# Performance work log

Hardware: AMD Instinct MI355X
Metric: run time of the kernel (lower is better)

The kernel has to match this reference:

```python
import jax, jax.numpy as jnp
import numpy as np

D_MODEL = 1024
N_HEADS = 16
HEAD_DIM = D_MODEL // N_HEADS
EPS = 1e-8  # torch F.cosine_similarity eps


def setup_inputs() -> dict:
    key = jax.random.key(0)
    ks = jax.random.split(key, 5)
    B, S = 2, 2048
    scale = 1.0 / np.sqrt(D_MODEL)
    return {
        "x": jax.random.normal(ks[0], (B, S, D_MODEL), dtype=jnp.float32),
        "W_q": jax.random.normal(ks[1], (D_MODEL, D_MODEL), dtype=jnp.float32) * scale,
        "W_k": jax.random.normal(ks[2], (D_MODEL, D_MODEL), dtype=jnp.float32) * scale,
        "W_v": jax.random.normal(ks[3], (D_MODEL, D_MODEL), dtype=jnp.float32) * scale,
        "W_o": jax.random.normal(ks[4], (D_MODEL, D_MODEL), dtype=jnp.float32) * scale,
    }


def _split_heads(t, B, S):
    # [B,S,D] -> [B,H,S,hd]
    return t.reshape(B, S, N_HEADS, HEAD_DIM).transpose(0, 2, 1, 3)


def reference(x, W_q, W_k, W_v, W_o):
    B, S, _ = x.shape
    Q = _split_heads(x @ W_q.T, B, S)
    K = _split_heads(x @ W_k.T, B, S)
    V = _split_heads(x @ W_v.T, B, S)

    # score[b,h,i,j] = cos_sim(q_i*k_j, ones) = sum_d(q*k) / (||q*k|| * sqrt(hd))
    num = jnp.einsum("bhid,bhjd->bhij", Q, K)
    # ||q_i \odot k_j||^2 = sum_d q^2 k^2, computed as a GEMM (no [B,H,S,S,D] blowup)
    norm_sq = jnp.einsum("bhid,bhjd->bhij", Q * Q, K * K)
    denom = jnp.maximum(jnp.sqrt(norm_sq), EPS) * jnp.sqrt(jnp.float32(HEAD_DIM))
    attn_scores = num / denom

    attn_weights = jax.nn.softmax(attn_scores, axis=-1)
    out = jnp.einsum("bhij,bhjd->bhid", attn_weights, V)
    out = out.transpose(0, 2, 1, 3).reshape(B, S, D_MODEL)
    out = out @ W_o.T
    return out, attn_weights
```

## Files before the change

### kernel.cpp

```cpp
#include <hip/hip_runtime.h>
#include <stdint.h>

typedef __bf16 bf16_t;
typedef __bf16 bf16x4_t __attribute__((ext_vector_type(4)));
typedef __bf16 bf16x8_t __attribute__((ext_vector_type(8)));
typedef float  f32x4_t  __attribute__((ext_vector_type(4)));

#define S_LEN 2048
#define DMODEL 1024
#define NHEAD 16
#define HDIM 64
#define MTOT 4096
#define NT 32
#define WBLK 4864

__device__ __forceinline__ f32x4_t mfma16(bf16x8_t a, bf16x8_t b, f32x4_t c){
  return __builtin_amdgcn_mfma_f32_16x16x32_bf16(a, b, c, 0, 0, 0);
}

__device__ __forceinline__ void gload_lds16(const bf16_t* g, bf16_t* l){
  __builtin_amdgcn_global_load_lds(
      (const __attribute__((address_space(1))) void*)(uintptr_t)g,
      (__attribute__((address_space(3))) void*)(uintptr_t)l,
      16, 0, 0);
}

template<int ROWS>
__device__ __forceinline__ void stage_tile(bf16_t* lds, const bf16_t* __restrict__ g,
                                           int ldg, int wid, int lane){
  const int rl = lane >> 3;
  const int cs = ((lane & 7) ^ rl) << 3;
#pragma unroll
  for (int it = 0; it < ROWS/32; ++it){
    const int chunk = it*4 + wid;
    gload_lds16(g + (size_t)(chunk*8 + rl)*ldg + cs, lds + chunk*512);
  }
}

__device__ __forceinline__ void stage_slice16(bf16_t* lds, const bf16_t* __restrict__ g,
                                              int lane){
  const int rl = lane >> 3;
  const int cs = ((lane & 7) ^ rl) << 3;
#pragma unroll
  for (int c = 0; c < 2; ++c)
    gload_lds16(g + (size_t)(c*8 + rl)*HDIM + cs, lds + c*512);
}

__device__ __forceinline__ void stage_v(bf16_t* lds, const bf16_t* __restrict__ g,
                                        int lane){
#pragma unroll
  for (int c = 0; c < 2; ++c)
    gload_lds16(g + (size_t)lane*64 + c*8, lds + c*512);
}

__device__ __forceinline__ bf16x8_t lds_read8(const bf16_t* t, int row, int ko){
  return *(const bf16x8_t*)&t[row*64 + (ko ^ ((row & 7) << 3))];
}

__device__ __forceinline__ bf16x8_t sq8(bf16x8_t v){
  bf16x8_t r;
#pragma unroll
  for (int i=0;i<8;i++){ float f = (float)v[i]; r[i] = (bf16_t)(f*f); }
  return r;
}

__global__ __launch_bounds__(256)
void vsa_cast_kernel(const float* __restrict__ src, bf16_t* __restrict__ dst, int n4){
  int i = blockIdx.x*256 + threadIdx.x;
  if (i >= n4) return;
  float4 v = ((const float4*)src)[i];
  bf16x4_t o = {(bf16_t)v.x,(bf16_t)v.y,(bf16_t)v.z,(bf16_t)v.w};
  ((bf16x4_t*)dst)[i] = o;
}

__global__ __launch_bounds__(256)
void vsa_qkv_kernel(const bf16_t* __restrict__ xb, const bf16_t* __restrict__ Wb,
                    bf16_t* __restrict__ Qb, bf16_t* __restrict__ Kb,
                    bf16_t* __restrict__ Vblk)
{
  __shared__ __align__(16) bf16_t Ah[128][64], Bh[128][64];
  const int z  = blockIdx.z;
  const int m0 = blockIdx.x * 128;
  const int n0 = blockIdx.y * 128;
  const int tid = threadIdx.x, lane = tid & 63, wid = tid >> 6;
  const int wr = (wid >> 1) * 64, wc = (wid & 1) * 64;
  const bf16_t* Wz = Wb + (size_t)z * (DMODEL*DMODEL);

  const f32x4_t zz = {0.f,0.f,0.f,0.f};
  f32x4_t acc[4][4];
#pragma unroll
  for (int i=0;i<4;i++)
#pragma unroll
    for (int j=0;j<4;j++) acc[i][j] = zz;

  for (int kt = 0; kt < 16; ++kt){
    const int k0 = kt * 64;
    stage_tile<128>(&Ah[0][0], xb + (size_t)m0*DMODEL + k0, DMODEL, wid, lane);
    stage_tile<128>(&Bh[0][0], Wz + (size_t)n0*DMODEL + k0, DMODEL, wid, lane);
    __syncthreads();
#pragma unroll
    for (int kk = 0; kk < 2; ++kk){
      const int ko = kk*32 + (lane>>4)*8;
      bf16x8_t ah[4], bh4[4];
#pragma unroll
      for (int i=0;i<4;i++){
        ah[i]  = lds_read8(&Ah[0][0], wr + i*16 + (lane&15), ko);
        bh4[i] = lds_read8(&Bh[0][0], wc + i*16 + (lane&15), ko);
      }
#pragma unroll
      for (int i=0;i<4;i++)
#pragma unroll
        for (int j=0;j<4;j++)
          acc[i][j] = mfma16(ah[i], bh4[j], acc[i][j]);
    }
    __syncthreads();
  }

#pragma unroll
  for (int i=0;i<4;i++)
#pragma unroll
    for (int j=0;j<4;j++)
#pragma unroll
      for (int r=0;r<4;r++){
        const int m = m0 + wr + i*16 + ((lane>>4)<<2) + r;
        const int n = n0 + wc + j*16 + (lane&15);
        const float q = acc[i][j][r];
        const int b = m >> 11, s = m & 2047, h = n >> 6, d = n & 63;
        const size_t bh_ = (size_t)b*NHEAD + h;
        if (z == 0){
          Qb[(bh_*S_LEN + s)*HDIM + d] = (bf16_t)q;
        } else if (z == 1){
          Kb[(bh_*S_LEN + s)*HDIM + d] = (bf16_t)q;
        } else {
          Vblk[bh_*(size_t)(S_LEN*HDIM) + (size_t)(s>>6)*4096 + d*64 + (s&63)] = (bf16_t)q;
        }
      }
}

__global__ __launch_bounds__(256, 4)
void vsa_attn_kernel(const bf16_t* __restrict__ Qb,
                     const bf16_t* __restrict__ Kb,
                     const bf16_t* __restrict__ Vblk,
                     float* __restrict__ Wout,
                     bf16_t* __restrict__ o1)
{
  __shared__ __align__(16) bf16_t smem[4*WBLK];
  __shared__ float lred[4][2][16];

  const int lin = blockIdx.x;
  const int xcd = lin & 7;
  const int idx = lin >> 3;
  const int qt  = idx & 63;
  const int bh  = xcd + 8*(idx >> 6);
  const int lane = threadIdx.x & 63, w = (int)(threadIdx.x >> 6);
  const int qr = lane & 15, cg = lane >> 4;

  const size_t base = (size_t)bh * (S_LEN*HDIM);
  const bf16_t* Kg = Kb   + base + (size_t)(w*16)*HDIM;
  const bf16_t* Vg = Vblk + base + w*16;

  bf16_t* Kbuf = smem + w*WBLK;
  bf16_t* Vbuf = Kbuf + 2048;
  bf16_t* Pbuf = Vbuf + 2048;

  bf16x8_t aq[2][2], aq2[2][2];
#pragma unroll
  for (int qh = 0; qh < 2; ++qh){
    const bf16_t* qrow = Qb + base + (size_t)(qt*32 + qh*16 + qr)*HDIM;
#pragma unroll
    for (int kk = 0; kk < 2; ++kk){
      aq[qh][kk] = *(const bf16x8_t*)(qrow + kk*32 + cg*8);
      bf16x8_t t;
#pragma unroll
      for (int e=0;e<8;e++){ float f = (float)aq[qh][kk][e]; t[e] = (bf16_t)(64.f*f*f); }
      aq2[qh][kk] = t;
    }
  }

  float lp[2][4] = {{0.f,0.f,0.f,0.f},{0.f,0.f,0.f,0.f}};
  stage_slice16(Kbuf, Kg, lane);
  for (int jt = 0; jt < NT; ++jt){
    const int nb = (jt+1) & (NT-1);
    __builtin_amdgcn_sched_barrier(0);
    stage_slice16(Kbuf + ((jt+1)&1)*1024, Kg + (size_t)nb*64*HDIM, lane);
    asm volatile("s_waitcnt vmcnt(2)" ::: "memory");
    __builtin_amdgcn_sched_barrier(0);
    const bf16_t* kb = Kbuf + (jt&1)*1024;
    bf16x8_t kf0  = lds_read8(kb, qr, cg*8), kf1 = lds_read8(kb, qr, 32+cg*8);
    bf16x8_t k2f0 = sq8(kf0),                k2f1 = sq8(kf1);
    f32x4_t nu[2], nr[2];
    __builtin_amdgcn_s_setprio(1);
#pragma unroll
    for (int qh = 0; qh < 2; ++qh){
      f32x4_t a = {0.f,0.f,0.f,0.f}, b = {0.f,0.f,0.f,0.f};
      a = mfma16(aq[qh][0],  kf0,  a); a = mfma16(aq[qh][1],  kf1,  a);
      b = mfma16(aq2[qh][0], k2f0, b); b = mfma16(aq2[qh][1], k2f1, b);
      nu[qh] = a; nr[qh] = b;
    }
    __builtin_amdgcn_s_setprio(0);
#pragma unroll
    for (int qh = 0; qh < 2; ++qh)
#pragma unroll
      for (int r=0;r<4;r++){
        const float s = nu[qh][r]*rsqrtf(fmaxf(nr[qh][r], 6.4e-15f));
        lp[qh][r] += __expf(s);
      }
  }

#pragma unroll
  for (int qh=0;qh<2;qh++)
#pragma unroll
    for (int r=0;r<4;r++){
      float l = lp[qh][r];
      l += __shfl_xor(l,1); l += __shfl_xor(l,2);
      l += __shfl_xor(l,4); l += __shfl_xor(l,8);
      lred[w][qh][cg*4+r] = l;
    }
  __syncthreads();
  float rl[2][4];
#pragma unroll
  for (int qh=0;qh<2;qh++)
#pragma unroll
    for (int r=0;r<4;r++)
      rl[qh][r] = 1.0f/(lred[0][qh][cg*4+r]+lred[1][qh][cg*4+r]
                       +lred[2][qh][cg*4+r]+lred[3][qh][cg*4+r]);

  const f32x4_t zz = {0.f,0.f,0.f,0.f};
  f32x4_t oacc[2][4];
#pragma unroll
  for (int qh=0;qh<2;qh++)
#pragma unroll
    for (int n=0;n<4;n++) oacc[qh][n] = zz;
  const size_t wb = (size_t)bh * S_LEN * S_LEN;
  const bf16x8_t zero8 = {};

  stage_v(Vbuf, Vg, lane);
  asm volatile("s_waitcnt vmcnt(0)" ::: "memory");
  __builtin_amdgcn_sched_barrier(0);

  for (int jt = 0; jt < NT; ++jt){
    const int nb = (jt+1) & (NT-1);
    __builtin_amdgcn_sched_barrier(0);
    stage_slice16(Kbuf + ((jt+1)&1)*1024, Kg + (size_t)nb*64*HDIM, lane);
    stage_v(Vbuf + ((jt+1)&1)*1024, Vg + (size_t)nb*4096, lane);
    asm volatile("s_waitcnt vmcnt(12)" ::: "memory");
    __builtin_amdgcn_sched_barrier(0);
    const bf16_t* kb = Kbuf + (jt&1)*1024;
    bf16x8_t kf0  = lds_read8(kb, qr, cg*8), kf1 = lds_read8(kb, qr, 32+cg*8);
    bf16x8_t k2f0 = sq8(kf0),                k2f1 = sq8(kf1);
    f32x4_t nu[2], nr[2];
    __builtin_amdgcn_s_setprio(1);
#pragma unroll
    for (int qh = 0; qh < 2; ++qh){
      f32x4_t a = {0.f,0.f,0.f,0.f}, b = {0.f,0.f,0.f,0.f};
      a = mfma16(aq[qh][0],  kf0,  a); a = mfma16(aq[qh][1],  kf1,  a);
      b = mfma16(aq2[qh][0], k2f0, b); b = mfma16(aq2[qh][1], k2f1, b);
      nu[qh] = a; nr[qh] = b;
    }
    __builtin_amdgcn_s_setprio(0);
#pragma unroll
    for (int qh = 0; qh < 2; ++qh)
#pragma unroll
      for (int r=0;r<4;r++){
        const float s = nu[qh][r]*rsqrtf(fmaxf(nr[qh][r], 6.4e-15f));
        const float wgt = __expf(s) * rl[qh][r];
        const int i = qt*32 + qh*16 + cg*4 + r;
        const int j = jt*64 + w*16 + qr;
        Wout[wb + (size_t)i*S_LEN + j] = wgt;
        Pbuf[qh*384 + (cg*4+r)*24 + qr] = (bf16_t)wgt;
      }
    asm volatile("s_waitcnt lgkmcnt(0)" ::: "memory");
    __builtin_amdgcn_sched_barrier(0);
    const int k0 = (cg & 1) * 8;
    bf16x8_t pa0 = (cg < 2) ? *(const bf16x8_t*)&Pbuf[      qr*24 + k0] : zero8;
    bf16x8_t pa1 = (cg < 2) ? *(const bf16x8_t*)&Pbuf[384 + qr*24 + k0] : zero8;
    const bf16_t* vbase = Vbuf + (jt&1)*1024 + (cg&1)*512;
    __builtin_amdgcn_s_setprio(1);
#pragma unroll
    for (int n=0;n<4;n++){
      bf16x8_t vb = *(const bf16x8_t*)&vbase[(n*16+qr)*8];
      oacc[0][n] = mfma16(pa0, vb, oacc[0][n]);
      oacc[1][n] = mfma16(pa1, vb, oacc[1][n]);
    }
    __builtin_amdgcn_s_setprio(0);
  }

  asm volatile("s_waitcnt vmcnt(0)" ::: "memory");
  __builtin_amdgcn_sched_barrier(0);
  float* Ow = (float*)Kbuf;
#pragma unroll
  for (int qh=0;qh<2;qh++)
#pragma unroll
    for (int n=0;n<4;n++)
#pragma unroll
      for (int r=0;r<4;r++)
        Ow[(qh*16+cg*4+r)*68 + n*16+qr] = oacc[qh][n][r];
  __syncthreads();
  {
    const int row = lane >> 1;
    const int jl  = (lane & 1)*8;
    float v[8];
#pragma unroll
    for (int e=0;e<8;e++) v[e] = 0.f;
#pragma unroll
    for (int ww=0; ww<4; ++ww){
      const float* Os = (const float*)(smem + ww*WBLK);
#pragma unroll
      for (int e=0;e<8;e++) v[e] += Os[row*68 + w*16 + jl + e];
    }
    const int b = bh >> 4, h = bh & 15;
    const int srow = qt*32 + row;
    const size_t o = ((size_t)b*S_LEN + srow)*DMODEL + (size_t)h*HDIM + w*16 + jl;
    bf16x8_t hv;
#pragma unroll
    for (int e=0;e<8;e++) hv[e] = (bf16_t)v[e];
    *(bf16x8_t*)(o1 + o) = hv;
  }
}

__global__ __launch_bounds__(256)
void vsa_oproj_kernel(const bf16_t* __restrict__ Ab, const bf16_t* __restrict__ Bb,
                      float* __restrict__ out)
{
  __shared__ __align__(16) bf16_t Ah[64][64], Bh[128][64];
  const int m0 = blockIdx.x * 64;
  const int n0 = blockIdx.y * 128;
  const int tid = threadIdx.x, lane = tid & 63, wid = tid >> 6;
  const int wc = wid * 32;

  const f32x4_t zz = {0.f,0.f,0.f,0.f};
  f32x4_t acc[4][2];
#pragma unroll
  for (int i=0;i<4;i++)
#pragma unroll
    for (int j=0;j<2;j++) acc[i][j] = zz;

  for (int kt = 0; kt < 16; ++kt){
    const int k0 = kt * 64;
    stage_tile<64> (&Ah[0][0], Ab + (size_t)m0*DMODEL + k0, DMODEL, wid, lane);
    stage_tile<128>(&Bh[0][0], Bb + (size_t)n0*DMODEL + k0, DMODEL, wid, lane);
    __syncthreads();
#pragma unroll
    for (int kk = 0; kk < 2; ++kk){
      const int ko = kk*32 + (lane>>4)*8;
      bf16x8_t ah[4], bh4[2];
#pragma unroll
      for (int i=0;i<4;i++)
        ah[i] = lds_read8(&Ah[0][0], i*16 + (lane&15), ko);
#pragma unroll
      for (int j=0;j<2;j++)
        bh4[j] = lds_read8(&Bh[0][0], wc + j*16 + (lane&15), ko);
#pragma unroll
      for (int i=0;i<4;i++)
#pragma unroll
        for (int j=0;j<2;j++)
          acc[i][j] = mfma16(ah[i], bh4[j], acc[i][j]);
    }
    __syncthreads();
  }

#pragma unroll
  for (int i=0;i<4;i++)
#pragma unroll
    for (int j=0;j<2;j++)
#pragma unroll
      for (int r=0;r<4;r++){
        const int m = m0 + i*16 + ((lane>>4)<<2) + r;
        const int n = n0 + wc + j*16 + (lane&15);
        out[(size_t)m*DMODEL + n] = acc[i][j][r];
      }
}

extern "C" void kernel_launch(void* const* d_in, const int* in_sizes, int n_in,
                              void* d_out, int out_size, void* d_ws, size_t ws_size,
                              hipStream_t stream)
{
  const float* x  = (const float*)d_in[0];
  const float* Wq = (const float*)d_in[1];
  const float* Wk = (const float*)d_in[2];
  const float* Wv = (const float*)d_in[3];
  const float* Wo = (const float*)d_in[4];
  float* out  = (float*)d_out;
  float* attw = out + (size_t)MTOT*DMODEL;

  bf16_t* ws = (bf16_t*)d_ws;
  const size_t C = 4194304;
  bf16_t* xb   = ws;
  bf16_t* Wb   = ws + C;
  bf16_t* Qb   = ws + 2*C;
  bf16_t* Kb   = ws + 3*C;
  bf16_t* Vblk = ws + 4*C;
  bf16_t* o1   = ws + 5*C;

  const int W1 = DMODEL*DMODEL;
  vsa_cast_kernel<<<(int)(C/1024), 256, 0, stream>>>(x,  xb, (int)(C/4));
  vsa_cast_kernel<<<W1/1024, 256, 0, stream>>>(Wq, Wb + 0*(size_t)W1, W1/4);
  vsa_cast_kernel<<<W1/1024, 256, 0, stream>>>(Wk, Wb + 1*(size_t)W1, W1/4);
  vsa_cast_kernel<<<W1/1024, 256, 0, stream>>>(Wv, Wb + 2*(size_t)W1, W1/4);
  vsa_cast_kernel<<<W1/1024, 256, 0, stream>>>(Wo, Wb + 3*(size_t)W1, W1/4);

  vsa_qkv_kernel<<<dim3(32, 8, 3), 256, 0, stream>>>(xb, Wb, Qb, Kb, Vblk);
  vsa_attn_kernel<<<dim3(2048), 256, 0, stream>>>(Qb, Kb, Vblk, attw, o1);
  vsa_oproj_kernel<<<dim3(64, 8), 256, 0, stream>>>(o1, Wb + 3*(size_t)W1, out);
}
```

Baseline: 308.7 us.

## Transpose score MFMA operands to vectorize weight stores and simplify row-sum reduction

Swaps the A/B operands of the score MFMAs so each lane holds four consecutive key columns for a single query row. The attention-weight output can then be written as 16-byte float4 stores and the P tile as 8-byte bf16x4 stores, instead of scattered scalar writes. The row-sum reduction shrinks to two cross-lane shuffles. Softmax normalization is folded into the exponent as exp2(s*log2e - log2(sum)), and the vmcnt wait threshold is adjusted to match the new number of outstanding loads. The risks are a small change in rounding and getting the wait count wrong for the new store pattern.

```diff
diff --git a/kernel.cpp b/kernel.cpp
--- a/kernel.cpp
+++ b/kernel.cpp
@@ -13,6 +13,7 @@
 #define MTOT 4096
 #define NT 32
 #define WBLK 4864
+#define LOG2E 1.4426950408889634f
 
 __device__ __forceinline__ f32x4_t mfma16(bf16x8_t a, bf16x8_t b, f32x4_t c){
   return __builtin_amdgcn_mfma_f32_16x16x32_bf16(a, b, c, 0, 0, 0);
@@ -177,7 +178,7 @@
     }
   }
 
-  float lp[2][4] = {{0.f,0.f,0.f,0.f},{0.f,0.f,0.f,0.f}};
+  float lp[2] = {0.f, 0.f};
   stage_slice16(Kbuf, Kg, lane);
   for (int jt = 0; jt < NT; ++jt){
     const int nb = (jt+1) & (NT-1);
@@ -193,8 +194,8 @@
 #pragma unroll
     for (int qh = 0; qh < 2; ++qh){
       f32x4_t a = {0.f,0.f,0.f,0.f}, b = {0.f,0.f,0.f,0.f};
-      a = mfma16(aq[qh][0],  kf0,  a); a = mfma16(aq[qh][1],  kf1,  a);
-      b = mfma16(aq2[qh][0], k2f0, b); b = mfma16(aq2[qh][1], k2f1, b);
+      a = mfma16(kf0,  aq[qh][0],  a); a = mfma16(kf1,  aq[qh][1],  a);
+      b = mfma16(k2f0, aq2[qh][0], b); b = mfma16(k2f1, aq2[qh][1], b);
       nu[qh] = a; nr[qh] = b;
     }
     __builtin_amdgcn_s_setprio(0);
@@ -203,27 +204,23 @@
 #pragma unroll
       for (int r=0;r<4;r++){
         const float s = nu[qh][r]*rsqrtf(fmaxf(nr[qh][r], 6.4e-15f));
-        lp[qh][r] += __expf(s);
+        lp[qh] += __builtin_amdgcn_exp2f(s * LOG2E);
       }
   }
 
 #pragma unroll
-  for (int qh=0;qh<2;qh++)
-#pragma unroll
-    for (int r=0;r<4;r++){
-      float l = lp[qh][r];
-      l += __shfl_xor(l,1); l += __shfl_xor(l,2);
-      l += __shfl_xor(l,4); l += __shfl_xor(l,8);
-      lred[w][qh][cg*4+r] = l;
-    }
+  for (int qh=0;qh<2;qh++){
+    float l = lp[qh];
+    l += __shfl_xor(l,16); l += __shfl_xor(l,32);
+    lred[w][qh][qr] = l;
+  }
   __syncthreads();
-  float rl[2][4];
-#pragma unroll
-  for (int qh=0;qh<2;qh++)
-#pragma unroll
-    for (int r=0;r<4;r++)
-      rl[qh][r] = 1.0f/(lred[0][qh][cg*4+r]+lred[1][qh][cg*4+r]
-                       +lred[2][qh][cg*4+r]+lred[3][qh][cg*4+r]);
+  float lrl2[2];
+#pragma unroll
+  for (int qh=0;qh<2;qh++){
+    const float lsum = lred[0][qh][qr]+lred[1][qh][qr]+lred[2][qh][qr]+lred[3][qh][qr];
+    lrl2[qh] = -__log2f(lsum);
+  }
 
   const f32x4_t zz = {0.f,0.f,0.f,0.f};
   f32x4_t oacc[2][4];
@@ -243,7 +240,7 @@
     __builtin_amdgcn_sched_barrier(0);
     stage_slice16(Kbuf + ((jt+1)&1)*1024, Kg + (size_t)nb*64*HDIM, lane);
     stage_v(Vbuf + ((jt+1)&1)*1024, Vg + (size_t)nb*4096, lane);
-    asm volatile("s_waitcnt vmcnt(12)" ::: "memory");
+    asm volatile("s_waitcnt vmcnt(6)" ::: "memory");
     __builtin_amdgcn_sched_barrier(0);
     const bf16_t* kb = Kbuf + (jt&1)*1024;
     bf16x8_t kf0  = lds_read8(kb, qr, cg*8), kf1 = lds_read8(kb, qr, 32+cg*8);
@@ -253,22 +250,24 @@
 #pragma unroll
     for (int qh = 0; qh < 2; ++qh){
       f32x4_t a = {0.f,0.f,0.f,0.f}, b = {0.f,0.f,0.f,0.f};
-      a = mfma16(aq[qh][0],  kf0,  a); a = mfma16(aq[qh][1],  kf1,  a);
-      b = mfma16(aq2[qh][0], k2f0, b); b = mfma16(aq2[qh][1], k2f1, b);
+      a = mfma16(kf0,  aq[qh][0],  a); a = mfma16(kf1,  aq[qh][1],  a);
+      b = mfma16(k2f0, aq2[qh][0], b); b = mfma16(k2f1, aq2[qh][1], b);
       nu[qh] = a; nr[qh] = b;
     }
     __builtin_amdgcn_s_setprio(0);
 #pragma unroll
-    for (int qh = 0; qh < 2; ++qh)
+    for (int qh = 0; qh < 2; ++qh){
+      f32x4_t wv;
 #pragma unroll
       for (int r=0;r<4;r++){
         const float s = nu[qh][r]*rsqrtf(fmaxf(nr[qh][r], 6.4e-15f));
-        const float wgt = __expf(s) * rl[qh][r];
-        const int i = qt*32 + qh*16 + cg*4 + r;
-        const int j = jt*64 + w*16 + qr;
-        Wout[wb + (size_t)i*S_LEN + j] = wgt;
-        Pbuf[qh*384 + (cg*4+r)*24 + qr] = (bf16_t)wgt;
+        wv[r] = __builtin_amdgcn_exp2f(__builtin_fmaf(s, LOG2E, lrl2[qh]));
       }
+      *(f32x4_t*)(Wout + wb + (size_t)(qt*32 + qh*16 + qr)*S_LEN
+                  + jt*64 + w*16 + cg*4) = wv;
+      bf16x4_t p4 = {(bf16_t)wv[0],(bf16_t)wv[1],(bf16_t)wv[2],(bf16_t)wv[3]};
+      *(bf16x4_t*)&Pbuf[qh*384 + qr*24 + cg*4] = p4;
+    }
     asm volatile("s_waitcnt lgkmcnt(0)" ::: "memory");
     __builtin_amdgcn_sched_barrier(0);
     const int k0 = (cg & 1) * 8;
```

Result: slower. 322.7 us (+4.5%).

## Triple-buffer K slices and load V directly into registers

Applied to the files above, without the earlier changes.

The K staging ring grows from double to triple buffering with a prefetch distance of two tiles in both attention passes. V is no longer staged through LDS: each lane loads its V fragments straight from global memory into registers, which frees LDS and shrinks the per-wave block. The aim is to hide global load latency better and drop the LDS round trip for V. In exchange, V loads are uncoalesced-ish direct global reads, and the explicit lgkmcnt wait before reading Pbuf was removed, which risks a race on the P write/read.

```diff
diff --git a/kernel.cpp b/kernel.cpp
--- a/kernel.cpp
+++ b/kernel.cpp
@@ -12,7 +12,7 @@
 #define HDIM 64
 #define MTOT 4096
 #define NT 32
-#define WBLK 4864
+#define WBLK 4352
 
 __device__ __forceinline__ f32x4_t mfma16(bf16x8_t a, bf16x8_t b, f32x4_t c){
   return __builtin_amdgcn_mfma_f32_16x16x32_bf16(a, b, c, 0, 0, 0);
@@ -44,13 +44,6 @@
 #pragma unroll
   for (int c = 0; c < 2; ++c)
     gload_lds16(g + (size_t)(c*8 + rl)*HDIM + cs, lds + c*512);
-}
-
-__device__ __forceinline__ void stage_v(bf16_t* lds, const bf16_t* __restrict__ g,
-                                        int lane){
-#pragma unroll
-  for (int c = 0; c < 2; ++c)
-    gload_lds16(g + (size_t)lane*64 + c*8, lds + c*512);
 }
 
 __device__ __forceinline__ bf16x8_t lds_read8(const bf16_t* t, int row, int ko){
@@ -156,12 +149,11 @@
   const int qr = lane & 15, cg = lane >> 4;
 
   const size_t base = (size_t)bh * (S_LEN*HDIM);
-  const bf16_t* Kg = Kb   + base + (size_t)(w*16)*HDIM;
-  const bf16_t* Vg = Vblk + base + w*16;
+  const bf16_t* Kg = Kb + base + (size_t)(w*16)*HDIM;
+  const bf16_t* Vl = Vblk + base + w*16 + (cg&1)*8 + (size_t)qr*64;
 
   bf16_t* Kbuf = smem + w*WBLK;
-  bf16_t* Vbuf = Kbuf + 2048;
-  bf16_t* Pbuf = Vbuf + 2048;
+  bf16_t* Pbuf = Kbuf + 3072;
 
   bf16x8_t aq[2][2], aq2[2][2];
 #pragma unroll
@@ -178,14 +170,15 @@
   }
 
   float lp[2][4] = {{0.f,0.f,0.f,0.f},{0.f,0.f,0.f,0.f}};
-  stage_slice16(Kbuf, Kg, lane);
+  stage_slice16(Kbuf,        Kg,                    lane);
+  stage_slice16(Kbuf + 1024, Kg + (size_t)64*HDIM,  lane);
+  int sst = 2, srd = 0;
   for (int jt = 0; jt < NT; ++jt){
-    const int nb = (jt+1) & (NT-1);
+    const int nb = (jt+2) & (NT-1);
+    stage_slice16(Kbuf + sst*1024, Kg + (size_t)nb*64*HDIM, lane);
+    asm volatile("s_waitcnt vmcnt(4)" ::: "memory");
     __builtin_amdgcn_sched_barrier(0);
-    stage_slice16(Kbuf + ((jt+1)&1)*1024, Kg + (size_t)nb*64*HDIM, lane);
-    asm volatile("s_waitcnt vmcnt(2)" ::: "memory");
-    __builtin_amdgcn_sched_barrier(0);
-    const bf16_t* kb = Kbuf + (jt&1)*1024;
+    const bf16_t* kb = Kbuf + srd*1024;
     bf16x8_t kf0  = lds_read8(kb, qr, cg*8), kf1 = lds_read8(kb, qr, 32+cg*8);
     bf16x8_t k2f0 = sq8(kf0),                k2f1 = sq8(kf1);
     f32x4_t nu[2], nr[2];
@@ -205,6 +198,8 @@
         const float s = nu[qh][r]*rsqrtf(fmaxf(nr[qh][r], 6.4e-15f));
         lp[qh][r] += __expf(s);
       }
+    sst = (sst==2) ? 0 : sst+1;
+    srd = (srd==2) ? 0 : srd+1;
   }
 
 #pragma unroll
@@ -234,18 +229,18 @@
   const size_t wb = (size_t)bh * S_LEN * S_LEN;
   const bf16x8_t zero8 = {};
 
-  stage_v(Vbuf, Vg, lane);
-  asm volatile("s_waitcnt vmcnt(0)" ::: "memory");
-  __builtin_amdgcn_sched_barrier(0);
-
   for (int jt = 0; jt < NT; ++jt){
-    const int nb = (jt+1) & (NT-1);
+    const int nb = (jt+2) & (NT-1);
+    bf16x8_t vreg[4];
+    {
+      const bf16_t* vt = Vl + (size_t)jt*4096;
+#pragma unroll
+      for (int n=0;n<4;n++) vreg[n] = *(const bf16x8_t*)(vt + n*1024);
+    }
+    stage_slice16(Kbuf + sst*1024, Kg + (size_t)nb*64*HDIM, lane);
+    asm volatile("s_waitcnt vmcnt(16)" ::: "memory");
     __builtin_amdgcn_sched_barrier(0);
-    stage_slice16(Kbuf + ((jt+1)&1)*1024, Kg + (size_t)nb*64*HDIM, lane);
-    stage_v(Vbuf + ((jt+1)&1)*1024, Vg + (size_t)nb*4096, lane);
-    asm volatile("s_waitcnt vmcnt(12)" ::: "memory");
-    __builtin_amdgcn_sched_barrier(0);
-    const bf16_t* kb = Kbuf + (jt&1)*1024;
+    const bf16_t* kb = Kbuf + srd*1024;
     bf16x8_t kf0  = lds_read8(kb, qr, cg*8), kf1 = lds_read8(kb, qr, 32+cg*8);
     bf16x8_t k2f0 = sq8(kf0),                k2f1 = sq8(kf1);
     f32x4_t nu[2], nr[2];
@@ -269,24 +264,21 @@
         Wout[wb + (size_t)i*S_LEN + j] = wgt;
         Pbuf[qh*384 + (cg*4+r)*24 + qr] = (bf16_t)wgt;
       }
-    asm volatile("s_waitcnt lgkmcnt(0)" ::: "memory");
-    __builtin_amdgcn_sched_barrier(0);
     const int k0 = (cg & 1) * 8;
     bf16x8_t pa0 = (cg < 2) ? *(const bf16x8_t*)&Pbuf[      qr*24 + k0] : zero8;
     bf16x8_t pa1 = (cg < 2) ? *(const bf16x8_t*)&Pbuf[384 + qr*24 + k0] : zero8;
-    const bf16_t* vbase = Vbuf + (jt&1)*1024 + (cg&1)*512;
     __builtin_amdgcn_s_setprio(1);
 #pragma unroll
     for (int n=0;n<4;n++){
-      bf16x8_t vb = *(const bf16x8_t*)&vbase[(n*16+qr)*8];
-      oacc[0][n] = mfma16(pa0, vb, oacc[0][n]);
-      oacc[1][n] = mfma16(pa1, vb, oacc[1][n]);
+      oacc[0][n] = mfma16(pa0, vreg[n], oacc[0][n]);
+      oacc[1][n] = mfma16(pa1, vreg[n], oacc[1][n]);
     }
     __builtin_amdgcn_s_setprio(0);
+    sst = (sst==2) ? 0 : sst+1;
+    srd = (srd==2) ? 0 : srd+1;
   }
 
   asm volatile("s_waitcnt vmcnt(0)" ::: "memory");
-  __builtin_amdgcn_sched_barrier(0);
   float* Ow = (float*)Kbuf;
 #pragma unroll
   for (int qh=0;qh<2;qh++)
```

Measured after the change: 376.4 us. +21.9%, slower.

## Shrink attention LDS footprint to fit five blocks per CU

Applied to the files above, without the earlier changes.

Cuts the per-wave LDS slice from 4864 to 4096 bf16 elements. It does this by single-buffering V, which is now loaded at the top of each iteration with its own vmcnt wait before the PV MFMAs. It also moves the row-sum reduction scratch into the P buffer region and packs the output staging with a 64-float stride read as vector loads. Launch bounds are raised to 5 blocks per CU so more blocks can be resident. The trade-off is that V loads are no longer prefetched a tile ahead, so V latency is exposed inside each iteration, and the unpadded 64-float stride may add LDS bank conflicts.

```diff
diff --git a/kernel.cpp b/kernel.cpp
--- a/kernel.cpp
+++ b/kernel.cpp
@@ -12,7 +12,7 @@
 #define HDIM 64
 #define MTOT 4096
 #define NT 32
-#define WBLK 4864
+#define WBLK 4096
 
 __device__ __forceinline__ f32x4_t mfma16(bf16x8_t a, bf16x8_t b, f32x4_t c){
   return __builtin_amdgcn_mfma_f32_16x16x32_bf16(a, b, c, 0, 0, 0);
@@ -137,7 +137,7 @@
       }
 }
 
-__global__ __launch_bounds__(256, 4)
+__global__ __launch_bounds__(256, 5)
 void vsa_attn_kernel(const bf16_t* __restrict__ Qb,
                      const bf16_t* __restrict__ Kb,
                      const bf16_t* __restrict__ Vblk,
@@ -145,7 +145,6 @@
                      bf16_t* __restrict__ o1)
 {
   __shared__ __align__(16) bf16_t smem[4*WBLK];
-  __shared__ float lred[4][2][16];
 
   const int lin = blockIdx.x;
   const int xcd = lin & 7;
@@ -161,7 +160,7 @@
 
   bf16_t* Kbuf = smem + w*WBLK;
   bf16_t* Vbuf = Kbuf + 2048;
-  bf16_t* Pbuf = Vbuf + 2048;
+  bf16_t* Pbuf = Kbuf + 3072;
 
   bf16x8_t aq[2][2], aq2[2][2];
 #pragma unroll
@@ -214,16 +213,21 @@
       float l = lp[qh][r];
       l += __shfl_xor(l,1); l += __shfl_xor(l,2);
       l += __shfl_xor(l,4); l += __shfl_xor(l,8);
-      lred[w][qh][cg*4+r] = l;
+      ((float*)Pbuf)[qh*16 + cg*4 + r] = l;
     }
   __syncthreads();
   float rl[2][4];
 #pragma unroll
   for (int qh=0;qh<2;qh++)
 #pragma unroll
-    for (int r=0;r<4;r++)
-      rl[qh][r] = 1.0f/(lred[0][qh][cg*4+r]+lred[1][qh][cg*4+r]
-                       +lred[2][qh][cg*4+r]+lred[3][qh][cg*4+r]);
+    for (int r=0;r<4;r++){
+      float lsum = 0.f;
+#pragma unroll
+      for (int ww=0; ww<4; ++ww)
+        lsum += ((const float*)(smem + ww*WBLK + 3072))[qh*16 + cg*4 + r];
+      rl[qh][r] = 1.0f/lsum;
+    }
+  __syncthreads();
 
   const f32x4_t zz = {0.f,0.f,0.f,0.f};
   f32x4_t oacc[2][4];
@@ -234,15 +238,11 @@
   const size_t wb = (size_t)bh * S_LEN * S_LEN;
   const bf16x8_t zero8 = {};
 
-  stage_v(Vbuf, Vg, lane);
-  asm volatile("s_waitcnt vmcnt(0)" ::: "memory");
-  __builtin_amdgcn_sched_barrier(0);
-
   for (int jt = 0; jt < NT; ++jt){
     const int nb = (jt+1) & (NT-1);
     __builtin_amdgcn_sched_barrier(0);
+    stage_v(Vbuf, Vg + (size_t)jt*4096, lane);
     stage_slice16(Kbuf + ((jt+1)&1)*1024, Kg + (size_t)nb*64*HDIM, lane);
-    stage_v(Vbuf + ((jt+1)&1)*1024, Vg + (size_t)nb*4096, lane);
     asm volatile("s_waitcnt vmcnt(12)" ::: "memory");
     __builtin_amdgcn_sched_barrier(0);
     const bf16_t* kb = Kbuf + (jt&1)*1024;
@@ -271,10 +271,12 @@
       }
     asm volatile("s_waitcnt lgkmcnt(0)" ::: "memory");
     __builtin_amdgcn_sched_barrier(0);
+    asm volatile("s_waitcnt vmcnt(10)" ::: "memory");
+    __builtin_amdgcn_sched_barrier(0);
     const int k0 = (cg & 1) * 8;
     bf16x8_t pa0 = (cg < 2) ? *(const bf16x8_t*)&Pbuf[      qr*24 + k0] : zero8;
     bf16x8_t pa1 = (cg < 2) ? *(const bf16x8_t*)&Pbuf[384 + qr*24 + k0] : zero8;
-    const bf16_t* vbase = Vbuf + (jt&1)*1024 + (cg&1)*512;
+    const bf16_t* vbase = Vbuf + (cg&1)*512;
     __builtin_amdgcn_s_setprio(1);
 #pragma unroll
     for (int n=0;n<4;n++){
@@ -286,7 +288,6 @@
   }
 
   asm volatile("s_waitcnt vmcnt(0)" ::: "memory");
-  __builtin_amdgcn_sched_barrier(0);
   float* Ow = (float*)Kbuf;
 #pragma unroll
   for (int qh=0;qh<2;qh++)
@@ -294,26 +295,26 @@
     for (int n=0;n<4;n++)
 #pragma unroll
       for (int r=0;r<4;r++)
-        Ow[(qh*16+cg*4+r)*68 + n*16+qr] = oacc[qh][n][r];
+        Ow[(qh*16+cg*4+r)*64 + n*16+qr] = oacc[qh][n][r];
   __syncthreads();
   {
     const int row = lane >> 1;
     const int jl  = (lane & 1)*8;
-    float v[8];
-#pragma unroll
-    for (int e=0;e<8;e++) v[e] = 0.f;
+    f32x4_t v0 = {0.f,0.f,0.f,0.f}, v1 = {0.f,0.f,0.f,0.f};
 #pragma unroll
     for (int ww=0; ww<4; ++ww){
-      const float* Os = (const float*)(smem + ww*WBLK);
-#pragma unroll
-      for (int e=0;e<8;e++) v[e] += Os[row*68 + w*16 + jl + e];
+      const float* Os = (const float*)(smem + ww*WBLK) + row*64 + w*16 + jl;
+      f32x4_t a = *(const f32x4_t*)Os;
+      f32x4_t b = *(const f32x4_t*)(Os + 4);
+#pragma unroll
+      for (int e=0;e<4;e++){ v0[e] += a[e]; v1[e] += b[e]; }
     }
     const int b = bh >> 4, h = bh & 15;
     const int srow = qt*32 + row;
     const size_t o = ((size_t)b*S_LEN + srow)*DMODEL + (size_t)h*HDIM + w*16 + jl;
     bf16x8_t hv;
 #pragma unroll
-    for (int e=0;e<8;e++) hv[e] = (bf16_t)v[e];
+    for (int e=0;e<4;e++){ hv[e] = (bf16_t)v0[e]; hv[4+e] = (bf16_t)v1[e]; }
     *(bf16x8_t*)(o1 + o) = hv;
   }
 }
```

Result: slower. 499.7 us (+61.8%).
